# Kernel optimization log

Measured on AMD Instinct MI355X. Metric: run time of the kernel, lower is better.

The kernel has to match this reference:

```python
import jax, jax.numpy as jnp
import numpy as np

B, H, S, D = 2, 8, 2048, 64
N_HASHES = 6
EPS = 1e-8


def setup_inputs() -> dict:
    key = jax.random.key(0)
    kq, kk, kv, kr = jax.random.split(key, 4)
    Q = jax.random.normal(kq, (B, H, S, D), dtype=jnp.float32)
    K = jax.random.normal(kk, (B, H, S, D), dtype=jnp.float32)
    V = jax.random.normal(kv, (B, H, S, D), dtype=jnp.float32)
    rotations = jax.random.normal(kr, (H, N_HASHES, D), dtype=jnp.float32)
    return {"Q": Q, "K": K, "V": V, "rotations": rotations}


def _buckets(X, rotations, powers):
    # X: [b,h,l,d] -> integer bucket id per position, [b,h,l]
    Xn = X / (jnp.linalg.norm(X, axis=-1, keepdims=True) + 1e-8)
    bits = jnp.einsum('bhld,hnd->bhln', Xn, rotations) > 0
    return jnp.sum(bits.astype(jnp.int32) * powers, axis=-1)


def reference(Q, K, V, rotations):
    n_hashes = rotations.shape[1]
    d = Q.shape[-1]
    powers = (2 ** jnp.arange(n_hashes)).astype(jnp.int32)
    q_buckets = _buckets(Q, rotations, powers)  # [b,h,sq]
    k_buckets = _buckets(K, rotations, powers)  # [b,h,sk]
    # queries only attend to keys whose full hash code matches exactly
    match = q_buckets[..., :, None] == k_buckets[..., None, :]  # [b,h,sq,sk]
    scores = jnp.einsum('bhqd,bhkd->bhqk', Q, K) / (d ** 0.5)
    row_has = jnp.any(match, axis=-1, keepdims=True)
    masked = jnp.where(match, scores, -jnp.inf)
    m = jnp.max(masked, axis=-1, keepdims=True)
    m = jnp.where(row_has, m, 0.0)  # avoid -inf for empty rows
    e = jnp.where(match, jnp.exp(scores - m), 0.0)
    weights = e / (jnp.sum(e, axis=-1, keepdims=True) + EPS)
    out = jnp.einsum('bhqk,bhkd->bhqd', weights, V)
    return out / n_hashes
```

## Files before the change

### kernel.cpp

```cpp
#include <hip/hip_runtime.h>
#include <math.h>


constexpr int S_LEN = 2048;
constexpr int D = 64;
constexpr int NHASH = 6;
constexpr int BH = 16;
constexpr int NB = 64;
constexpr int QPAD = 4;
constexpr int PADQ = S_LEN + (QPAD - 1) * NB;
constexpr int NGRP = PADQ / QPAD;
constexpr int NBLK = NGRP / 4;
constexpr int KCH = 32;

__global__ __launch_bounds__(256) void lsh_buckets2(const float* __restrict__ Q,
                                                    const float* __restrict__ K,
                                                    const float* __restrict__ rot,
                                                    int* __restrict__ qb,
                                                    int* __restrict__ kb) {
    const int gw   = (blockIdx.x * 256 + threadIdx.x) >> 6;
    const int lane = threadIdx.x & 63;
    const bool isK = gw >= BH * S_LEN;
    const int wid  = isK ? gw - BH * S_LEN : gw;
    const float* X = isK ? K : Q;
    int* dst       = isK ? kb : qb;
    const int h    = (wid >> 11) & 7;

    const float x  = X[(size_t)wid * D + lane];
    const float* r = rot + (size_t)h * NHASH * D + lane;
    float p0 = x * r[0 * D], p1 = x * r[1 * D], p2 = x * r[2 * D];
    float p3 = x * r[3 * D], p4 = x * r[4 * D], p5 = x * r[5 * D];
#pragma unroll
    for (int off = 32; off >= 1; off >>= 1) {
        p0 += __shfl_xor(p0, off, 64);
        p1 += __shfl_xor(p1, off, 64);
        p2 += __shfl_xor(p2, off, 64);
        p3 += __shfl_xor(p3, off, 64);
        p4 += __shfl_xor(p4, off, 64);
        p5 += __shfl_xor(p5, off, 64);
    }
    int bucket = (p0 > 0.f ? 1 : 0) | (p1 > 0.f ? 2 : 0) | (p2 > 0.f ? 4 : 0) |
                 (p3 > 0.f ? 8 : 0) | (p4 > 0.f ? 16 : 0) | (p5 > 0.f ? 32 : 0);
    if (lane == 0) dst[wid] = bucket;
}

__global__ __launch_bounds__(256) void lsh_sortfuse_bh(const int* __restrict__ qbuckets,
                                                       const int* __restrict__ kbuckets,
                                                       int* __restrict__ q_plist,
                                                       int* __restrict__ k_list) {
    __shared__ int hist[NB];
    __shared__ int cur[NB];
    __shared__ int kst[NB], kcnt[NB];
    __shared__ int qst[NB];
    __shared__ int total;
    const int bh  = blockIdx.x;
    const int tid = threadIdx.x;

    if (tid < NB) hist[tid] = 0;
    __syncthreads();
    int myk[8];
#pragma unroll
    for (int i = 0; i < 8; ++i) {
        myk[i] = kbuckets[bh * S_LEN + i * 256 + tid];
        atomicAdd(&hist[myk[i]], 1);
    }
    __syncthreads();
    if (tid < NB) {
        const int cnt = hist[tid];
        int x = cnt;
#pragma unroll
        for (int off = 1; off < 64; off <<= 1) {
            const int y = __shfl_up(x, off, 64);
            if (tid >= off) x += y;
        }
        kst[tid]  = x - cnt;
        kcnt[tid] = cnt;
        cur[tid]  = x - cnt;
    }
    __syncthreads();
    {
        int* klp = k_list + bh * S_LEN;
#pragma unroll
        for (int i = 0; i < 8; ++i) {
            const int b    = myk[i];
            const int slot = atomicAdd(&cur[b], 1);
            klp[slot] = i * 256 + tid;
        }
    }
    __syncthreads();

    if (tid < NB) hist[tid] = 0;
    __syncthreads();
    int myq[8];
#pragma unroll
    for (int i = 0; i < 8; ++i) {
        myq[i] = qbuckets[bh * S_LEN + i * 256 + tid];
        atomicAdd(&hist[myq[i]], 1);
    }
    __syncthreads();
    if (tid < NB) {
        const int cnt = hist[tid];
        const int v   = (cnt + QPAD - 1) & ~(QPAD - 1);
        int x = v;
#pragma unroll
        for (int off = 1; off < 64; off <<= 1) {
            const int y = __shfl_up(x, off, 64);
            if (tid >= off) x += y;
        }
        qst[tid] = x - v;
        cur[tid] = x - v;
        if (tid == 63) total = x;
    }
    __syncthreads();

    int* qp = q_plist + bh * PADQ;
    if (tid < NB) {
        const int cnt    = hist[tid];
        const int padded = (cnt + QPAD - 1) & ~(QPAD - 1);
        const int sent   = 0xFFFF | (kcnt[tid] << 16);
        for (int t = qst[tid] + cnt; t < qst[tid] + padded; ++t) qp[t] = sent;
    }
    for (int t = total + tid; t < PADQ; t += 256) qp[t] = -1;
#pragma unroll
    for (int i = 0; i < 8; ++i) {
        const int b    = myq[i];
        const int slot = atomicAdd(&cur[b], 1);
        const int pos  = slot & 3;
        int e = i * 256 + tid;
        if (pos == 0)      e |= kst[b] << 16;
        else if (pos == 1) e |= kcnt[b] << 16;
        qp[slot] = e;
    }
}

__global__ __launch_bounds__(256) void lsh_attn_d(const float* __restrict__ Q,
                                                  const float* __restrict__ K,
                                                  const float* __restrict__ V,
                                                  const int* __restrict__ q_plist,
                                                  const int* __restrict__ k_list,
                                                  float* __restrict__ out) {
    __shared__ float qlds[4][QPAD][64];
    __shared__ float wbuf[4][QPAD][KCH];
    __shared__ int   kbuf[4][KCH];

    const int wv   = threadIdx.x >> 6;
    const int lane = threadIdx.x & 63;
    const int h    = lane >> 5;
    const int kk   = lane & 31;
    const int w    = blockIdx.x;
    const int bh   = (w & 7) + 8 * ((w >> 3) & 1);
    const int blk  = w >> 4;
    const int grp  = blk * 4 + wv;

    const int* pl = q_plist + bh * PADQ + 4 * grp;
    const int e0 = __builtin_amdgcn_readfirstlane(pl[0]);
    if ((e0 & 0xFFFF) == 0xFFFF) return;
    const int e1 = __builtin_amdgcn_readfirstlane(pl[1]);
    const int e2 = __builtin_amdgcn_readfirstlane(pl[2]);
    const int e3 = __builtin_amdgcn_readfirstlane(pl[3]);

    const int q0 = e0 & 0xFFFF;
    const int ks = (unsigned)e0 >> 16;
    const int nk = (unsigned)e1 >> 16;
    const int t1 = e1 & 0xFFFF, t2 = e2 & 0xFFFF, t3 = e3 & 0xFFFF;
    const bool v1 = t1 != 0xFFFF, v2 = t2 != 0xFFFF, v3 = t3 != 0xFFFF;
    const int q1 = v1 ? t1 : q0;
    const int q2 = v2 ? t2 : q0;
    const int q3 = v3 ? t3 : q0;

    float* outb = out + (size_t)bh * S_LEN * D;
    if (nk == 0) {
        outb[(size_t)q0 * D + lane] = 0.0f;
        if (v1) outb[(size_t)q1 * D + lane] = 0.0f;
        if (v2) outb[(size_t)q2 * D + lane] = 0.0f;
        if (v3) outb[(size_t)q3 * D + lane] = 0.0f;
        return;
    }

    const int* kl   = k_list + bh * S_LEN + ks;
    const float* Kb = K + (size_t)bh * S_LEN * D;
    const float* Vb = V + (size_t)bh * S_LEN * D;
    const float* Qb = Q + (size_t)bh * S_LEN * D;

    qlds[wv][0][lane] = Qb[(size_t)q0 * D + lane];
    qlds[wv][1][lane] = Qb[(size_t)q1 * D + lane];
    qlds[wv][2][lane] = Qb[(size_t)q2 * D + lane];
    qlds[wv][3][lane] = Qb[(size_t)q3 * D + lane];

    float l0 = 0.f, l1 = 0.f;
    float acc[QPAD] = {0.f, 0.f, 0.f, 0.f};

    for (int c = 0; c * KCH < nk; ++c) {
        const int cnk  = min(KCH, nk - c * KCH);
        const int kidx = kl[c * KCH + min(kk, cnk - 1)];
        const float* krow = Kb + (size_t)kidx * D + h * 32;

        float4 kv[8];
#pragma unroll
        for (int i = 0; i < 8; ++i) kv[i] = *(const float4*)(krow + i * 4);

        float s[QPAD];
#pragma unroll
        for (int j = 0; j < QPAD; ++j) {
            const float* qj = &qlds[wv][j][h * 32];
            float sj = 0.f;
#pragma unroll
            for (int i = 0; i < 8; ++i) {
                const float4 qv = *(const float4*)(qj + i * 4);
                sj += qv.x * kv[i].x + qv.y * kv[i].y + qv.z * kv[i].z + qv.w * kv[i].w;
            }
            s[j] = sj;
        }
        s[0] += __shfl_xor(s[0], 32, 64);
        s[1] += __shfl_xor(s[1], 32, 64);
        s[2] += __shfl_xor(s[2], 32, 64);
        s[3] += __shfl_xor(s[3], 32, 64);

        const bool kvalid = kk < cnk;
        const float sa = h ? s[2] : s[0];
        const float sb = h ? s[3] : s[1];
        const float ea = kvalid ? __expf(sa * 0.125f) : 0.f;
        const float eb = kvalid ? __expf(sb * 0.125f) : 0.f;
        l0 += ea;
        l1 += eb;
        wbuf[wv][2 * h + 0][kk] = ea;
        wbuf[wv][2 * h + 1][kk] = eb;
        if (h == 0) kbuf[wv][kk] = kidx;

        const int ng = (cnk + 3) >> 2;
        for (int g = 0; g < ng; ++g) {
            const int4 kx = *(const int4*)&kbuf[wv][g * 4];
            const float vx = Vb[(size_t)kx.x * D + lane];
            const float vy = Vb[(size_t)kx.y * D + lane];
            const float vz = Vb[(size_t)kx.z * D + lane];
            const float vw = Vb[(size_t)kx.w * D + lane];
            const float4 eA = *(const float4*)&wbuf[wv][0][g * 4];
            const float4 eB = *(const float4*)&wbuf[wv][1][g * 4];
            const float4 eC = *(const float4*)&wbuf[wv][2][g * 4];
            const float4 eD = *(const float4*)&wbuf[wv][3][g * 4];
            acc[0] += eA.x * vx + eA.y * vy + eA.z * vz + eA.w * vw;
            acc[1] += eB.x * vx + eB.y * vy + eB.z * vz + eB.w * vw;
            acc[2] += eC.x * vx + eC.y * vy + eC.z * vz + eC.w * vw;
            acc[3] += eD.x * vx + eD.y * vy + eD.z * vz + eD.w * vw;
        }
    }

#pragma unroll
    for (int off = 16; off >= 1; off >>= 1) {
        l0 += __shfl_xor(l0, off, 64);
        l1 += __shfl_xor(l1, off, 64);
    }
    const float o0 = __shfl_xor(l0, 32, 64);
    const float o1 = __shfl_xor(l1, 32, 64);
    const float lq0 = h ? o0 : l0;
    const float lq1 = h ? o1 : l1;
    const float lq2 = h ? l0 : o0;
    const float lq3 = h ? l1 : o1;

    const float inv6 = 1.0f / 6.0f;
    outb[(size_t)q0 * D + lane] = acc[0] / (lq0 + 1e-8f) * inv6;
    if (v1) outb[(size_t)q1 * D + lane] = acc[1] / (lq1 + 1e-8f) * inv6;
    if (v2) outb[(size_t)q2 * D + lane] = acc[2] / (lq2 + 1e-8f) * inv6;
    if (v3) outb[(size_t)q3 * D + lane] = acc[3] / (lq3 + 1e-8f) * inv6;
}

extern "C" void kernel_launch(void* const* d_in, const int* in_sizes, int n_in,
                              void* d_out, int out_size, void* d_ws, size_t ws_size,
                              hipStream_t stream) {
    const float* Q   = (const float*)d_in[0];
    const float* K   = (const float*)d_in[1];
    const float* V   = (const float*)d_in[2];
    const float* rot = (const float*)d_in[3];
    float* out = (float*)d_out;

    char* ws = (char*)d_ws;
    int* q_buckets = (int*)(ws);
    int* k_buckets = (int*)(ws + 131072);
    int* k_list    = (int*)(ws + 262144);
    int* q_plist   = (int*)(ws + 393216);

    lsh_buckets2<<<2 * BH * S_LEN / 4, 256, 0, stream>>>(Q, K, rot, q_buckets, k_buckets);
    lsh_sortfuse_bh<<<BH, 256, 0, stream>>>(q_buckets, k_buckets, q_plist, k_list);
    lsh_attn_d<<<NBLK * BH, 256, 0, stream>>>(Q, K, V, q_plist, k_list, out);
}
```

Before: 72.81 us.

## Map one key per lane over full head dim, read Q directly from global

Restructures the attention kernel so each of 64 lanes handles one full key (64-wide dot product) instead of splitting each key's head dimension across two half-waves. Chunks widen from 32 to 64 keys, which removes the cross-half shuffles and lane-select logic for scores and row sums. Q rows are now read straight from global memory (wave-uniform addresses, likely scalar or broadcast loads) instead of being staged in LDS. In exchange, each lane reads an entire 256-byte K row, so the K gather is less coalesced, and register pressure may rise.

```diff
diff --git a/kernel.cpp b/kernel.cpp
--- a/kernel.cpp
+++ b/kernel.cpp
@@ -11,7 +11,6 @@
 constexpr int PADQ = S_LEN + (QPAD - 1) * NB;
 constexpr int NGRP = PADQ / QPAD;
 constexpr int NBLK = NGRP / 4;
-constexpr int KCH = 32;
 
 __global__ __launch_bounds__(256) void lsh_buckets2(const float* __restrict__ Q,
                                                     const float* __restrict__ K,
@@ -133,24 +132,20 @@
     }
 }
 
-__global__ __launch_bounds__(256) void lsh_attn_d(const float* __restrict__ Q,
+__global__ __launch_bounds__(256) void lsh_attn_g(const float* __restrict__ Q,
                                                   const float* __restrict__ K,
                                                   const float* __restrict__ V,
                                                   const int* __restrict__ q_plist,
                                                   const int* __restrict__ k_list,
                                                   float* __restrict__ out) {
-    __shared__ float qlds[4][QPAD][64];
-    __shared__ float wbuf[4][QPAD][KCH];
-    __shared__ int   kbuf[4][KCH];
+    __shared__ float wbuf[4][QPAD][64];
+    __shared__ int   kbuf[4][64];
 
     const int wv   = threadIdx.x >> 6;
     const int lane = threadIdx.x & 63;
-    const int h    = lane >> 5;
-    const int kk   = lane & 31;
     const int w    = blockIdx.x;
     const int bh   = (w & 7) + 8 * ((w >> 3) & 1);
-    const int blk  = w >> 4;
-    const int grp  = blk * 4 + wv;
+    const int grp  = (w >> 4) * 4 + wv;
 
     const int* pl = q_plist + bh * PADQ + 4 * grp;
     const int e0 = __builtin_amdgcn_readfirstlane(pl[0]);
@@ -177,91 +172,79 @@
         return;
     }
 
-    const int* kl   = k_list + bh * S_LEN + ks;
-    const float* Kb = K + (size_t)bh * S_LEN * D;
-    const float* Vb = V + (size_t)bh * S_LEN * D;
-    const float* Qb = Q + (size_t)bh * S_LEN * D;
-
-    qlds[wv][0][lane] = Qb[(size_t)q0 * D + lane];
-    qlds[wv][1][lane] = Qb[(size_t)q1 * D + lane];
-    qlds[wv][2][lane] = Qb[(size_t)q2 * D + lane];
-    qlds[wv][3][lane] = Qb[(size_t)q3 * D + lane];
-
-    float l0 = 0.f, l1 = 0.f;
-    float acc[QPAD] = {0.f, 0.f, 0.f, 0.f};
-
-    for (int c = 0; c * KCH < nk; ++c) {
-        const int cnk  = min(KCH, nk - c * KCH);
-        const int kidx = kl[c * KCH + min(kk, cnk - 1)];
-        const float* krow = Kb + (size_t)kidx * D + h * 32;
-
-        float4 kv[8];
-#pragma unroll
-        for (int i = 0; i < 8; ++i) kv[i] = *(const float4*)(krow + i * 4);
-
-        float s[QPAD];
-#pragma unroll
-        for (int j = 0; j < QPAD; ++j) {
-            const float* qj = &qlds[wv][j][h * 32];
-            float sj = 0.f;
-#pragma unroll
-            for (int i = 0; i < 8; ++i) {
-                const float4 qv = *(const float4*)(qj + i * 4);
-                sj += qv.x * kv[i].x + qv.y * kv[i].y + qv.z * kv[i].z + qv.w * kv[i].w;
-            }
-            s[j] = sj;
-        }
-        s[0] += __shfl_xor(s[0], 32, 64);
-        s[1] += __shfl_xor(s[1], 32, 64);
-        s[2] += __shfl_xor(s[2], 32, 64);
-        s[3] += __shfl_xor(s[3], 32, 64);
-
-        const bool kvalid = kk < cnk;
-        const float sa = h ? s[2] : s[0];
-        const float sb = h ? s[3] : s[1];
-        const float ea = kvalid ? __expf(sa * 0.125f) : 0.f;
-        const float eb = kvalid ? __expf(sb * 0.125f) : 0.f;
-        l0 += ea;
-        l1 += eb;
-        wbuf[wv][2 * h + 0][kk] = ea;
-        wbuf[wv][2 * h + 1][kk] = eb;
-        if (h == 0) kbuf[wv][kk] = kidx;
+    const int* kl     = k_list + bh * S_LEN + ks;
+    const float* Kb   = K + (size_t)bh * S_LEN * D;
+    const float* Vb   = V + (size_t)bh * S_LEN * D;
+    const float* qr0  = Q + ((size_t)bh * S_LEN + q0) * D;
+    const float* qr1  = Q + ((size_t)bh * S_LEN + q1) * D;
+    const float* qr2  = Q + ((size_t)bh * S_LEN + q2) * D;
+    const float* qr3  = Q + ((size_t)bh * S_LEN + q3) * D;
+
+    float l0 = 0.f, l1 = 0.f, l2 = 0.f, l3 = 0.f;
+    float acc0 = 0.f, acc1 = 0.f, acc2 = 0.f, acc3 = 0.f;
+
+    for (int c = 0; c * 64 < nk; ++c) {
+        const int cnk  = min(64, nk - c * 64);
+        const int kidx = kl[c * 64 + min(lane, cnk - 1)];
+        const float* krow = Kb + (size_t)kidx * D;
+
+        float s0 = 0.f, s1 = 0.f, s2 = 0.f, s3 = 0.f;
+#pragma unroll
+        for (int d4 = 0; d4 < 16; ++d4) {
+            const float4 kv = *(const float4*)(krow + d4 * 4);
+            const float4 a  = *(const float4*)(qr0 + d4 * 4);
+            const float4 b  = *(const float4*)(qr1 + d4 * 4);
+            const float4 cq = *(const float4*)(qr2 + d4 * 4);
+            const float4 dq = *(const float4*)(qr3 + d4 * 4);
+            s0 += a.x * kv.x + a.y * kv.y + a.z * kv.z + a.w * kv.w;
+            s1 += b.x * kv.x + b.y * kv.y + b.z * kv.z + b.w * kv.w;
+            s2 += cq.x * kv.x + cq.y * kv.y + cq.z * kv.z + cq.w * kv.w;
+            s3 += dq.x * kv.x + dq.y * kv.y + dq.z * kv.z + dq.w * kv.w;
+        }
+
+        const bool kvalid = lane < cnk;
+        const float ea = kvalid ? __expf(s0 * 0.125f) : 0.f;
+        const float eb = kvalid ? __expf(s1 * 0.125f) : 0.f;
+        const float ec = kvalid ? __expf(s2 * 0.125f) : 0.f;
+        const float ed = kvalid ? __expf(s3 * 0.125f) : 0.f;
+        l0 += ea; l1 += eb; l2 += ec; l3 += ed;
+        wbuf[wv][0][lane] = ea;
+        wbuf[wv][1][lane] = eb;
+        wbuf[wv][2][lane] = ec;
+        wbuf[wv][3][lane] = ed;
+        kbuf[wv][lane]    = kidx;
 
         const int ng = (cnk + 3) >> 2;
         for (int g = 0; g < ng; ++g) {
-            const int4 kx = *(const int4*)&kbuf[wv][g * 4];
-            const float vx = Vb[(size_t)kx.x * D + lane];
-            const float vy = Vb[(size_t)kx.y * D + lane];
-            const float vz = Vb[(size_t)kx.z * D + lane];
-            const float vw = Vb[(size_t)kx.w * D + lane];
+            const int4   kk = *(const int4*)&kbuf[wv][g * 4];
             const float4 eA = *(const float4*)&wbuf[wv][0][g * 4];
             const float4 eB = *(const float4*)&wbuf[wv][1][g * 4];
             const float4 eC = *(const float4*)&wbuf[wv][2][g * 4];
             const float4 eD = *(const float4*)&wbuf[wv][3][g * 4];
-            acc[0] += eA.x * vx + eA.y * vy + eA.z * vz + eA.w * vw;
-            acc[1] += eB.x * vx + eB.y * vy + eB.z * vz + eB.w * vw;
-            acc[2] += eC.x * vx + eC.y * vy + eC.z * vz + eC.w * vw;
-            acc[3] += eD.x * vx + eD.y * vy + eD.z * vz + eD.w * vw;
-        }
-    }
-
-#pragma unroll
-    for (int off = 16; off >= 1; off >>= 1) {
+            const float vx = Vb[(size_t)kk.x * D + lane];
+            const float vy = Vb[(size_t)kk.y * D + lane];
+            const float vz = Vb[(size_t)kk.z * D + lane];
+            const float vw = Vb[(size_t)kk.w * D + lane];
+            acc0 += eA.x * vx + eA.y * vy + eA.z * vz + eA.w * vw;
+            acc1 += eB.x * vx + eB.y * vy + eB.z * vz + eB.w * vw;
+            acc2 += eC.x * vx + eC.y * vy + eC.z * vz + eC.w * vw;
+            acc3 += eD.x * vx + eD.y * vy + eD.z * vz + eD.w * vw;
+        }
+    }
+
+#pragma unroll
+    for (int off = 32; off >= 1; off >>= 1) {
         l0 += __shfl_xor(l0, off, 64);
         l1 += __shfl_xor(l1, off, 64);
-    }
-    const float o0 = __shfl_xor(l0, 32, 64);
-    const float o1 = __shfl_xor(l1, 32, 64);
-    const float lq0 = h ? o0 : l0;
-    const float lq1 = h ? o1 : l1;
-    const float lq2 = h ? l0 : o0;
-    const float lq3 = h ? l1 : o1;
+        l2 += __shfl_xor(l2, off, 64);
+        l3 += __shfl_xor(l3, off, 64);
+    }
 
     const float inv6 = 1.0f / 6.0f;
-    outb[(size_t)q0 * D + lane] = acc[0] / (lq0 + 1e-8f) * inv6;
-    if (v1) outb[(size_t)q1 * D + lane] = acc[1] / (lq1 + 1e-8f) * inv6;
-    if (v2) outb[(size_t)q2 * D + lane] = acc[2] / (lq2 + 1e-8f) * inv6;
-    if (v3) outb[(size_t)q3 * D + lane] = acc[3] / (lq3 + 1e-8f) * inv6;
+    outb[(size_t)q0 * D + lane] = acc0 / (l0 + 1e-8f) * inv6;
+    if (v1) outb[(size_t)q1 * D + lane] = acc1 / (l1 + 1e-8f) * inv6;
+    if (v2) outb[(size_t)q2 * D + lane] = acc2 / (l2 + 1e-8f) * inv6;
+    if (v3) outb[(size_t)q3 * D + lane] = acc3 / (l3 + 1e-8f) * inv6;
 }
 
 extern "C" void kernel_launch(void* const* d_in, const int* in_sizes, int n_in,
@@ -281,5 +264,5 @@
 
     lsh_buckets2<<<2 * BH * S_LEN / 4, 256, 0, stream>>>(Q, K, rot, q_buckets, k_buckets);
     lsh_sortfuse_bh<<<BH, 256, 0, stream>>>(q_buckets, k_buckets, q_plist, k_list);
-    lsh_attn_d<<<NBLK * BH, 256, 0, stream>>>(Q, K, V, q_plist, k_list, out);
-}
+    lsh_attn_g<<<NBLK * BH, 256, 0, stream>>>(Q, K, V, q_plist, k_list, out);
+}
```

Measured after the change: 75.84 us. +4.2%, slower.
